# Kernel optimization log

Measured on AMD Instinct MI355X. Metric: run time of the kernel, lower is better.

Reference implementation:

```python
import jax, jax.numpy as jnp
import numpy as np

B, T, N, D, H, F, L, V = 4, 512, 1024, 384, 8, 1536, 6, 8000
HD = D // H


def _pe(t, d):
    pos = np.arange(t)[:, None].astype(np.float32)
    div = np.exp(np.arange(0, d, 2).astype(np.float32) * (-np.log(10000.0) / d))
    pe = np.zeros((t, d), np.float32)
    pe[:, 0::2] = np.sin(pos * div)
    pe[:, 1::2] = np.cos(pos * div)
    return jnp.asarray(pe)


def _ln(x, g, b, eps=1e-5):
    m = jnp.mean(x, -1, keepdims=True)
    v = jnp.mean((x - m) ** 2, -1, keepdims=True)
    return (x - m) * jax.lax.rsqrt(v + eps) * g + b


def _mha(xq, xkv, qw, qb, kw, kb, vw, vb, ow, ob, causal):
    Bq, Tq, Dm = xq.shape
    Nk = xkv.shape[1]

    def proj(x, w, b):
        return (x @ w + b).reshape(x.shape[0], x.shape[1], H, HD).transpose(0, 2, 1, 3)

    q, k, v = proj(xq, qw, qb), proj(xkv, kw, kb), proj(xkv, vw, vb)
    s = jnp.einsum('bhtd,bhnd->bhtn', q, k) * (HD ** -0.5)
    if causal:  # triu(ones(T, T_total), diagonal=1) since T_total == T (no cache)
        mask = jnp.triu(jnp.ones((Tq, Nk), bool), 1)
        s = jnp.where(mask, -jnp.inf, s)
    p = jax.nn.softmax(s, -1)
    o = jnp.einsum('bhtn,bhnd->bhtd', p, v).transpose(0, 2, 1, 3).reshape(Bq, Tq, Dm)
    return o @ ow + ob


def setup_inputs() -> dict:
    key = jax.random.key(0)
    ks = iter(jax.random.split(key, 40))
    w = lambda shape, s=0.02: jax.random.normal(next(ks), shape, jnp.float32) * s
    inp = {
        'encoder_out': jax.random.normal(next(ks), (B, N, D), jnp.float32),
        'emb': w((V, D)),
    }
    for p in ('sa', 'ca'):
        for n in ('q', 'k', 'v', 'o'):
            inp[f'{p}_{n}w'] = w((L, D, D))
            inp[f'{p}_{n}b'] = jnp.zeros((L, D), jnp.float32)
    for n in ('ln1', 'ln2', 'ln3'):
        inp[f'{n}_g'] = jnp.ones((L, D), jnp.float32)
        inp[f'{n}_b'] = jnp.zeros((L, D), jnp.float32)
    inp['ffn_w1'] = w((L, D, F)); inp['ffn_b1'] = jnp.zeros((L, F), jnp.float32)
    inp['ffn_w2'] = w((L, F, D)); inp['ffn_b2'] = jnp.zeros((L, D), jnp.float32)
    inp['on_g'] = jnp.ones((D,), jnp.float32); inp['on_b'] = jnp.zeros((D,), jnp.float32)
    inp['out_w'] = w((D, V)); inp['out_b'] = jnp.zeros((V,), jnp.float32)
    inp['target_ids'] = jax.random.randint(next(ks), (B, T), 0, V)
    return inp


def _forward(encoder_out, emb, sa_qw, sa_qb, sa_kw, sa_kb, sa_vw, sa_vb, sa_ow, sa_ob,
             ca_qw, ca_qb, ca_kw, ca_kb, ca_vw, ca_vb, ca_ow, ca_ob,
             ln1_g, ln1_b, ln2_g, ln2_b, ln3_g, ln3_b,
             ffn_w1, ffn_b1, ffn_w2, ffn_b2, on_g, on_b, out_w, out_b, target_ids):
    x = emb[target_ids] + _pe(T, D)[None]  # [B,T,D]
    for i in range(L):
        a = _mha(x, x, sa_qw[i], sa_qb[i], sa_kw[i], sa_kb[i], sa_vw[i], sa_vb[i], sa_ow[i], sa_ob[i], True)
        x = _ln(x + a, ln1_g[i], ln1_b[i])
        c = _mha(x, encoder_out, ca_qw[i], ca_qb[i], ca_kw[i], ca_kb[i], ca_vw[i], ca_vb[i], ca_ow[i], ca_ob[i], False)
        x = _ln(x + c, ln2_g[i], ln2_b[i])
        h = jax.nn.gelu(x @ ffn_w1[i] + ffn_b1[i], approximate=False) @ ffn_w2[i] + ffn_b2[i]
        x = _ln(x + h, ln3_g[i], ln3_b[i])
    x = _ln(x, on_g, on_b)
    return x @ out_w + out_b  # logits [B,T,V]


def reference(encoder_out, emb, sa_qw, sa_qb, sa_kw, sa_kb, sa_vw, sa_vb, sa_ow, sa_ob,
              ca_qw, ca_qb, ca_kw, ca_kb, ca_vw, ca_vb, ca_ow, ca_ob,
              ln1_g, ln1_b, ln2_g, ln2_b, ln3_g, ln3_b,
              ffn_w1, ffn_b1, ffn_w2, ffn_b2, on_g, on_b, out_w, out_b, target_ids):
    return _forward(encoder_out, emb, sa_qw, sa_qb, sa_kw, sa_kb, sa_vw, sa_vb, sa_ow, sa_ob,
                    ca_qw, ca_qb, ca_kw, ca_kb, ca_vw, ca_vb, ca_ow, ca_ob,
                    ln1_g, ln1_b, ln2_g, ln2_b, ln3_g, ln3_b,
                    ffn_w1, ffn_b1, ffn_w2, ffn_b2, on_g, on_b, out_w, out_b, target_ids)
```

## Files before the change

### kernel.cpp

```cpp
#include <hip/hip_runtime.h>
#include <hip/hip_bf16.h>
#include <math.h>

typedef __hip_bfloat16 bf16;
typedef __attribute__((ext_vector_type(8))) short short8;
typedef __attribute__((ext_vector_type(4))) float f32x4;
typedef __attribute__((ext_vector_type(4))) unsigned short us4;

#define Bc 4
#define Tc 512
#define Nc 1024
#define Dc 384
#define Hc 8
#define Fc 1536
#define Lc 6
#define Vc 8000
#define HDc 48

__device__ __forceinline__ float ldsel(const void* p, long long i, int isbf) {
  return isbf ? __bfloat162float(((const bf16*)p)[i]) : ((const float*)p)[i];
}
__device__ __forceinline__ void stsel(void* p, long long i, float v, int isbf) {
  if (isbf) ((bf16*)p)[i] = __float2bfloat16(v);
  else      ((float*)p)[i] = v;
}
__device__ __forceinline__ unsigned short f2bf(float x) {
  unsigned int u = __float_as_uint(x);
  return (unsigned short)((u + 0x7fffu + ((u >> 16) & 1u)) >> 16);
}

__global__ void detect_kernel(const unsigned int* __restrict__ g,
                              int* __restrict__ flag) {
  if (threadIdx.x == 0 && blockIdx.x == 0)
    *flag = (g[0] == 0x3F803F80u) ? 1 : 0;
}

__global__ __launch_bounds__(256) void wt_kernel(
    const void* __restrict__ in, bf16* __restrict__ out, int K, int N,
    long long outStride, const int* __restrict__ flagp) {
  const int isbf = *flagp;
  __shared__ float t[32][33];
  const long long cin = (long long)blockIdx.z * K * N;
  const long long cout = (long long)blockIdx.z * outStride;
  const int n0 = blockIdx.x * 32, k0 = blockIdx.y * 32;
  const int tx = threadIdx.x, ty = threadIdx.y;
#pragma unroll
  for (int r = 0; r < 4; ++r)
    t[ty * 4 + r][tx] =
        ldsel(in, cin + (long long)(k0 + ty * 4 + r) * N + n0 + tx, isbf);
  __syncthreads();
#pragma unroll
  for (int r = 0; r < 4; ++r)
    out[cout + (long long)(n0 + ty * 4 + r) * K + k0 + tx] =
        __float2bfloat16(t[tx][ty * 4 + r]);
}

__global__ __launch_bounds__(256) void cvt_kernel(
    const void* __restrict__ in, bf16* __restrict__ out,
    const int* __restrict__ flagp) {
  const int isbf = *flagp;
  const long long i = ((long long)blockIdx.x * 256 + threadIdx.x) * 4;
  if (isbf) {
    *(us4*)((unsigned short*)out + i) = *(const us4*)((const unsigned short*)in + i);
  } else {
    float4 v = *(const float4*)((const float*)in + i);
    unsigned short* o = (unsigned short*)out + i;
    o[0] = f2bf(v.x); o[1] = f2bf(v.y); o[2] = f2bf(v.z); o[3] = f2bf(v.w);
  }
}

__global__ __launch_bounds__(256) void bfuse_kernel(
    const void* __restrict__ b0, const void* __restrict__ b1,
    const void* __restrict__ b2, float* __restrict__ out, int nseg,
    const int* __restrict__ flagp) {
  const int isbf = *flagp;
  const int i = blockIdx.x;
  for (int n = threadIdx.x; n < Dc; n += 256) {
    out[(long long)i * nseg * Dc + n] = ldsel(b0, (long long)i * Dc + n, isbf);
    if (nseg > 1)
      out[(long long)i * nseg * Dc + Dc + n] = ldsel(b1, (long long)i * Dc + n, isbf);
    if (nseg > 2)
      out[(long long)i * nseg * Dc + 2 * Dc + n] = ldsel(b2, (long long)i * Dc + n, isbf);
  }
}

template <int BN>
__global__ __launch_bounds__(256) void mgemm128_kernel(
    const bf16* __restrict__ A, const bf16* __restrict__ Bt, long long bOff,
    const void* __restrict__ bias, long long biasOff, void* __restrict__ C,
    int M, int N, int K, int cMode, int act, int biasBf,
    const int* __restrict__ flagp) {
  constexpr int RN = BN / 32;
  const int isbf = *flagp;
  const int cbf = (cMode == 2) ? isbf : cMode;
  const int bbf = (biasBf == 2) ? isbf : biasBf;

  __shared__ __align__(16) unsigned short As[128][72];
  __shared__ __align__(16) unsigned short Bs[BN][72];

  const int tid = threadIdx.x;
  const int m0 = blockIdx.x * 128, n0 = blockIdx.y * BN;
  const int lane = tid & 63, wv = tid >> 6;
  const int wm = wv >> 1, wn = wv & 1;
  const int fr = lane & 15;
  const int fk = (lane >> 4) * 8;

  const int ar = tid >> 3;
  const int ac = (tid & 7) * 8;
  const bf16* Ap = A + (long long)(m0 + ar) * K + ac;
  const bf16* Bp = Bt + bOff + (long long)(n0 + ar) * K + ac;

  short8 pa[4], pb[RN * 2];
#pragma unroll
  for (int r = 0; r < 4; ++r) pa[r] = *(const short8*)(Ap + r * 32 * K);
#pragma unroll
  for (int r = 0; r < RN * 2; ++r) pb[r] = *(const short8*)(Bp + r * 32 * K);

  f32x4 acc[4][RN] = {};

  for (int k0 = 0; k0 < K; k0 += 64) {
#pragma unroll
    for (int r = 0; r < 4; ++r) *(short8*)(&As[ar + 32 * r][ac]) = pa[r];
#pragma unroll
    for (int r = 0; r < RN * 2; ++r) *(short8*)(&Bs[ar + 32 * r][ac]) = pb[r];
    __syncthreads();
    if (k0 + 64 < K) {
#pragma unroll
      for (int r = 0; r < 4; ++r)
        pa[r] = *(const short8*)(Ap + r * 32 * K + k0 + 64);
#pragma unroll
      for (int r = 0; r < RN * 2; ++r)
        pb[r] = *(const short8*)(Bp + r * 32 * K + k0 + 64);
    }
#pragma unroll
    for (int ks = 0; ks < 64; ks += 32) {
      short8 af[4];
#pragma unroll
      for (int mi = 0; mi < 4; ++mi)
        af[mi] = *(const short8*)(&As[wm * 64 + mi * 16 + fr][ks + fk]);
      short8 bg[RN];
#pragma unroll
      for (int ni = 0; ni < RN; ++ni)
        bg[ni] = *(const short8*)(&Bs[wn * (BN / 2) + ni * 16 + fr][ks + fk]);
#pragma unroll
      for (int mi = 0; mi < 4; ++mi)
#pragma unroll
        for (int ni = 0; ni < RN; ++ni)
          acc[mi][ni] =
              __builtin_amdgcn_mfma_f32_16x16x32_bf16(af[mi], bg[ni], acc[mi][ni], 0, 0, 0);
    }
    __syncthreads();
  }

#pragma unroll
  for (int ni = 0; ni < RN; ++ni) {
    const int col = n0 + wn * (BN / 2) + ni * 16 + fr;
    const float bv = bias ? ldsel(bias, biasOff + col, bbf) : 0.f;
#pragma unroll
    for (int mi = 0; mi < 4; ++mi) {
#pragma unroll
      for (int q = 0; q < 4; ++q) {
        const int row = m0 + wm * 64 + mi * 16 + (lane >> 4) * 4 + q;
        float v = acc[mi][ni][q] + bv;
        if (act == 1) v = 0.5f * v * (1.f + erff(v * 0.70710678118654752f));
        stsel(C, (long long)row * N + col, v, cbf);
      }
    }
  }
}

__global__ __launch_bounds__(256) void mgemm_kernel(
    const bf16* __restrict__ A, const void* __restrict__ B, long long bOff,
    const void* __restrict__ bias, long long biasOff, void* __restrict__ C,
    int M, int N, int K, int cMode, int act, int biasBf, int bT,
    const float* __restrict__ POm, const float* __restrict__ Mst,
    const float* __restrict__ Lst, int comb, const int* __restrict__ flagp) {
  const int isbf = *flagp;
  const int cbf = (cMode == 2) ? isbf : cMode;
  const int bbf = (biasBf == 2) ? isbf : biasBf;

  __shared__ __align__(16) unsigned short As[64][72];
  __shared__ __align__(16) unsigned short Bs[64][72];

  const int tid = threadIdx.x;
  const int m0 = blockIdx.x * 64, n0 = blockIdx.y * 64;
  const int lane = tid & 63, wv = tid >> 6;
  const int fr = lane & 15;
  const int fk = (lane >> 4) * 8;

  const int sr = tid >> 2;
  const int sk = (tid & 3) * 16;

  f32x4 acc[4] = {};

  if (bT == 0 && comb == 0) {
    const bf16* Bp = (const bf16*)B + bOff;
    const bf16* Ar = A + (long long)(m0 + sr) * K + sk;
    const bf16* Br = Bp + (long long)(n0 + sr) * K + sk;
    short8 a0 = *(const short8*)(Ar);
    short8 a1 = *(const short8*)(Ar + 8);
    short8 b0 = *(const short8*)(Br);
    short8 b1 = *(const short8*)(Br + 8);
    for (int k0 = 0; k0 < K; k0 += 64) {
      *(short8*)(&As[sr][sk]) = a0;
      *(short8*)(&As[sr][sk + 8]) = a1;
      *(short8*)(&Bs[sr][sk]) = b0;
      *(short8*)(&Bs[sr][sk + 8]) = b1;
      __syncthreads();
      if (k0 + 64 < K) {
        a0 = *(const short8*)(Ar + k0 + 64);
        a1 = *(const short8*)(Ar + k0 + 72);
        b0 = *(const short8*)(Br + k0 + 64);
        b1 = *(const short8*)(Br + k0 + 72);
      }
#pragma unroll
      for (int ks = 0; ks < 64; ks += 32) {
        short8 a = *(const short8*)(&As[16 * wv + fr][ks + fk]);
#pragma unroll
        for (int j = 0; j < 4; ++j) {
          short8 b = *(const short8*)(&Bs[16 * j + fr][ks + fk]);
          acc[j] = __builtin_amdgcn_mfma_f32_16x16x32_bf16(a, b, acc[j], 0, 0, 0);
        }
      }
      __syncthreads();
    }
  } else {
    const int bk = tid >> 2;
    const int bn = (tid & 3) * 16;
    for (int k0 = 0; k0 < K; k0 += 64) {
      if (comb) {
        const int gm = m0 + sr;
        const int gk = k0 + sk;
        const int hh = gk / 48;
        const int bb = gm >> 9, tt = gm & 511;
        const int mi = ((bb << 3) + hh) * 512 + tt;
        const float ma = Mst[mi], mb2 = Mst[16384 + mi];
        const float la = Lst[mi], lb2 = Lst[16384 + mi];
        const float MM = fmaxf(ma, mb2);
        float w0 = exp2f(ma - MM), w1 = exp2f(mb2 - MM);
        const float invL = 1.f / (w0 * la + w1 * lb2);
        w0 *= invL; w1 *= invL;
        const float* p0 = POm + (long long)gm * Dc + gk;
        const float* p1 = POm + (long long)(2048 + gm) * Dc + gk;
#pragma unroll
        for (int e = 0; e < 16; e += 4) {
          float4 x0 = *(const float4*)(p0 + e);
          float4 x1 = *(const float4*)(p1 + e);
          As[sr][sk + e + 0] = f2bf(w0 * x0.x + w1 * x1.x);
          As[sr][sk + e + 1] = f2bf(w0 * x0.y + w1 * x1.y);
          As[sr][sk + e + 2] = f2bf(w0 * x0.z + w1 * x1.z);
          As[sr][sk + e + 3] = f2bf(w0 * x0.w + w1 * x1.w);
        }
      } else {
        const long long off = (long long)(m0 + sr) * K + k0 + sk;
        const short8* p = (const short8*)(A + off);
        *(short8*)(&As[sr][sk]) = p[0];
        *(short8*)(&As[sr][sk + 8]) = p[1];
      }
      if (bT == 0) {
        const long long off = bOff + (long long)(n0 + sr) * K + k0 + sk;
        const short8* p = (const short8*)((const bf16*)B + off);
        *(short8*)(&Bs[sr][sk]) = p[0];
        *(short8*)(&Bs[sr][sk + 8]) = p[1];
      } else {
        const long long off = bOff + (long long)(k0 + bk) * N + n0 + bn;
        if (isbf) {
          const short8* p = (const short8*)((const bf16*)B + off);
          short8 v0 = p[0], v1 = p[1];
#pragma unroll
          for (int j = 0; j < 8; ++j) {
            Bs[bn + j][bk] = (unsigned short)v0[j];
            Bs[bn + 8 + j][bk] = (unsigned short)v1[j];
          }
        } else {
          const float4* p = (const float4*)((const float*)B + off);
          float4 f0 = p[0], f1 = p[1], f2 = p[2], f3 = p[3];
          Bs[bn + 0][bk] = f2bf(f0.x);  Bs[bn + 1][bk] = f2bf(f0.y);
          Bs[bn + 2][bk] = f2bf(f0.z);  Bs[bn + 3][bk] = f2bf(f0.w);
          Bs[bn + 4][bk] = f2bf(f1.x);  Bs[bn + 5][bk] = f2bf(f1.y);
          Bs[bn + 6][bk] = f2bf(f1.z);  Bs[bn + 7][bk] = f2bf(f1.w);
          Bs[bn + 8][bk] = f2bf(f2.x);  Bs[bn + 9][bk] = f2bf(f2.y);
          Bs[bn + 10][bk] = f2bf(f2.z); Bs[bn + 11][bk] = f2bf(f2.w);
          Bs[bn + 12][bk] = f2bf(f3.x); Bs[bn + 13][bk] = f2bf(f3.y);
          Bs[bn + 14][bk] = f2bf(f3.z); Bs[bn + 15][bk] = f2bf(f3.w);
        }
      }
      __syncthreads();
#pragma unroll
      for (int ks = 0; ks < 64; ks += 32) {
        short8 a = *(const short8*)(&As[16 * wv + fr][ks + fk]);
#pragma unroll
        for (int j = 0; j < 4; ++j) {
          short8 b = *(const short8*)(&Bs[16 * j + fr][ks + fk]);
          acc[j] = __builtin_amdgcn_mfma_f32_16x16x32_bf16(a, b, acc[j], 0, 0, 0);
        }
      }
      __syncthreads();
    }
  }

#pragma unroll
  for (int j = 0; j < 4; ++j) {
    const int col = n0 + 16 * j + fr;
    float bv = bias ? ldsel(bias, biasOff + col, bbf) : 0.f;
#pragma unroll
    for (int q = 0; q < 4; ++q) {
      const int row = m0 + 16 * wv + (lane >> 4) * 4 + q;
      float v = acc[j][q] + bv;
      if (act == 1) v = 0.5f * v * (1.f + erff(v * 0.70710678118654752f));
      stsel(C, (long long)row * N + col, v, cbf);
    }
  }
}

__global__ __launch_bounds__(256) void mattn_kernel(
    const bf16* __restrict__ Qb, int ldq, const bf16* __restrict__ Kb,
    const bf16* __restrict__ Vb, int ldkv, int kvRows,
    float* __restrict__ PO, float* __restrict__ Mb, float* __restrict__ Lb,
    int Nk, int causal) {
  const int bh = blockIdx.y;
  const int b = bh >> 3, h = bh & 7;
  const int row0 = blockIdx.x * 64;
  const int z = blockIdx.z;
  const int tid = threadIdx.x;
  const int lane = tid & 63, wv = tid >> 6;
  const int fr = lane & 15, g = lane >> 4;
  const int fk = g * 8, g4 = g * 4;
  const int rbase = row0 + wv * 16 + g4;

  __shared__ __align__(16) unsigned short Ks[64][72];
  __shared__ __align__(16) unsigned short Vt[48][72];
  __shared__ __align__(16) unsigned short Ps[4][16][72];

  for (int i = tid; i < 64 * 16; i += 256) Ks[i >> 4][48 + (i & 15)] = 0;

  const int qrow = row0 + wv * 16 + fr;
  const bf16* Qp = Qb + (long long)(b * Tc + qrow) * ldq + h * HDc;
  short8 q0 = *(const short8*)(Qp + fk);
  short8 q1 = {};
  if (g < 2) q1 = *(const short8*)(Qp + 32 + fk);

  const bf16* Kp = Kb + (long long)b * kvRows * ldkv + h * HDc;
  const bf16* Vp = Vb + (long long)b * kvRows * ldkv + h * HDc;

  const int c0 = tid, c1 = 256 + tid;
  const int r0 = c0 / 6, o0 = (c0 % 6) * 8;
  const int r1 = c1 / 6, o1 = (c1 % 6) * 8;
  const bool has1 = (tid < 128);

  const int nT = causal ? (blockIdx.x + 1) : (Nk >> 6);
  const int tlo = (nT * z) >> 1, thi = (nT * (z + 1)) >> 1;

  float m[4] = {-3e38f, -3e38f, -3e38f, -3e38f};
  float l[4] = {0.f, 0.f, 0.f, 0.f};
  f32x4 oa[3] = {};

  short8 kA = {}, vA = {}, kB = {}, vB = {};
  if (tlo < thi) {
    const long long nb = (long long)tlo * 64;
    kA = *(const short8*)(Kp + (nb + r0) * ldkv + o0);
    vA = *(const short8*)(Vp + (nb + r0) * ldkv + o0);
    if (has1) {
      kB = *(const short8*)(Kp + (nb + r1) * ldkv + o1);
      vB = *(const short8*)(Vp + (nb + r1) * ldkv + o1);
    }
  }

  const float scale = 0.20823509f;

  for (int t = tlo; t < thi; ++t) {
    *(short8*)&Ks[r0][o0] = kA;
#pragma unroll
    for (int j = 0; j < 8; ++j) Vt[o0 + j][r0] = (unsigned short)vA[j];
    if (has1) {
      *(short8*)&Ks[r1][o1] = kB;
#pragma unroll
      for (int j = 0; j < 8; ++j) Vt[o1 + j][r1] = (unsigned short)vB[j];
    }
    __syncthreads();

    if (t + 1 < thi) {
      const long long nb = (long long)(t + 1) * 64;
      kA = *(const short8*)(Kp + (nb + r0) * ldkv + o0);
      vA = *(const short8*)(Vp + (nb + r0) * ldkv + o0);
      if (has1) {
        kB = *(const short8*)(Kp + (nb + r1) * ldkv + o1);
        vB = *(const short8*)(Vp + (nb + r1) * ldkv + o1);
      }
    }

    f32x4 s[4] = {};
#pragma unroll
    for (int tt = 0; tt < 4; ++tt) {
      short8 b0 = *(const short8*)&Ks[16 * tt + fr][fk];
      short8 b1 = *(const short8*)&Ks[16 * tt + fr][32 + fk];
      s[tt] = __builtin_amdgcn_mfma_f32_16x16x32_bf16(q0, b0, s[tt], 0, 0, 0);
      s[tt] = __builtin_amdgcn_mfma_f32_16x16x32_bf16(q1, b1, s[tt], 0, 0, 0);
    }

    const int n0 = t * 64;
#pragma unroll
    for (int tt = 0; tt < 4; ++tt) {
      const int n = n0 + 16 * tt + fr;
#pragma unroll
      for (int q = 0; q < 4; ++q) {
        float v = s[tt][q] * scale;
        if (causal && n > rbase + q) v = -3e38f;
        s[tt][q] = v;
      }
    }

#pragma unroll
    for (int q = 0; q < 4; ++q) {
      float tm = fmaxf(fmaxf(s[0][q], s[1][q]), fmaxf(s[2][q], s[3][q]));
      tm = fmaxf(tm, __shfl_xor(tm, 1, 64));
      tm = fmaxf(tm, __shfl_xor(tm, 2, 64));
      tm = fmaxf(tm, __shfl_xor(tm, 4, 64));
      tm = fmaxf(tm, __shfl_xor(tm, 8, 64));
      const float mn = fmaxf(m[q], tm);
      const float f = exp2f(m[q] - mn);
      float rs = 0.f;
#pragma unroll
      for (int tt = 0; tt < 4; ++tt) {
        float p = exp2f(s[tt][q] - mn);
        s[tt][q] = p;
        rs += p;
      }
      rs += __shfl_xor(rs, 1, 64);
      rs += __shfl_xor(rs, 2, 64);
      rs += __shfl_xor(rs, 4, 64);
      rs += __shfl_xor(rs, 8, 64);
      l[q] = l[q] * f + rs;
      m[q] = mn;
      oa[0][q] *= f;
      oa[1][q] *= f;
      oa[2][q] *= f;
    }

#pragma unroll
    for (int tt = 0; tt < 4; ++tt)
#pragma unroll
      for (int q = 0; q < 4; ++q)
        Ps[wv][g4 + q][16 * tt + fr] = f2bf(s[tt][q]);

#pragma unroll
    for (int ks = 0; ks < 64; ks += 32) {
      short8 a = *(const short8*)&Ps[wv][fr][ks + fk];
#pragma unroll
      for (int jd = 0; jd < 3; ++jd) {
        short8 bv = *(const short8*)&Vt[16 * jd + fr][ks + fk];
        oa[jd] = __builtin_amdgcn_mfma_f32_16x16x32_bf16(a, bv, oa[jd], 0, 0, 0);
      }
    }
    __syncthreads();
  }

#pragma unroll
  for (int q = 0; q < 4; ++q) {
    float* pp = PO + (long long)(z * (Bc * Tc) + b * Tc + rbase + q) * Dc + h * HDc;
#pragma unroll
    for (int jd = 0; jd < 3; ++jd) pp[16 * jd + fr] = oa[jd][q];
    if (fr == 0) {
      const int mi = z * (Bc * Hc * Tc) + (bh << 9) + rbase + q;
      Mb[mi] = m[q];
      Lb[mi] = l[q];
    }
  }
}

__global__ __launch_bounds__(256) void lnw_kernel(
    const float* __restrict__ X, const float* __restrict__ R,
    const void* __restrict__ g, const void* __restrict__ bta, long long gOff,
    void* __restrict__ Y, int yMode, bf16* __restrict__ Yb,
    const int* __restrict__ flagp) {
  const int isbf = *flagp;
  const long long row = blockIdx.x * 4 + (threadIdx.x >> 6);
  const int lane = threadIdx.x & 63;
  const float* xr = X + row * Dc;
  const float* rr = R ? R + row * Dc : nullptr;
  float v[6];
  float s = 0.f, s2 = 0.f;
#pragma unroll
  for (int j = 0; j < 6; ++j) {
    const int d = lane + 64 * j;
    float x = xr[d] + (rr ? rr[d] : 0.f);
    v[j] = x; s += x; s2 += x * x;
  }
#pragma unroll
  for (int k = 1; k < 64; k <<= 1) {
    s += __shfl_xor(s, k, 64);
    s2 += __shfl_xor(s2, k, 64);
  }
  const float mean = s * (1.f / 384.f);
  const float var = s2 * (1.f / 384.f) - mean * mean;
  const float rstd = rsqrtf(var + 1e-5f);
  const long long yo = row * Dc;
#pragma unroll
  for (int j = 0; j < 6; ++j) {
    const int d = lane + 64 * j;
    float y = (v[j] - mean) * rstd * ldsel(g, gOff + d, isbf) +
              ldsel(bta, gOff + d, isbf);
    stsel(Y, yo + d, y, yMode);
    if (Yb) Yb[yo + d] = __float2bfloat16(y);
  }
}

__global__ __launch_bounds__(384) void embed_kernel(
    const void* __restrict__ emb, const int* __restrict__ ids,
    float* __restrict__ X, bf16* __restrict__ Xb,
    const int* __restrict__ flagp) {
  const int isbf = *flagp;
  long long row = blockIdx.x;
  int t = (int)(row % Tc);
  int d = threadIdx.x;
  int id = ids[row];
  float e = ldsel(emb, (long long)id * Dc + d, isbf);
  int i2 = d & ~1;
  float div = expf((float)i2 * (-9.210340371976184f / 384.f));
  float ang = (float)t * div;
  float pe = (d & 1) ? cosf(ang) : sinf(ang);
  float v = e + pe;
  X[row * Dc + d] = v;
  Xb[row * Dc + d] = __float2bfloat16(v);
}

extern "C" void kernel_launch(void* const* d_in, const int* in_sizes, int n_in,
                              void* d_out, int out_size, void* d_ws,
                              size_t ws_size, hipStream_t stream) {
  (void)in_sizes; (void)n_in; (void)out_size;

  const void* enc = d_in[0];
  const void* emb = d_in[1];
  const void* sa_w[4]; const void* sa_b[4];
  for (int j = 0; j < 4; ++j) { sa_w[j] = d_in[2 + 2 * j]; sa_b[j] = d_in[3 + 2 * j]; }
  const void* ca_w[4]; const void* ca_b[4];
  for (int j = 0; j < 4; ++j) { ca_w[j] = d_in[10 + 2 * j]; ca_b[j] = d_in[11 + 2 * j]; }
  const void* ln_g[3]; const void* ln_b[3];
  for (int j = 0; j < 3; ++j) { ln_g[j] = d_in[18 + 2 * j]; ln_b[j] = d_in[19 + 2 * j]; }
  const void* fw1 = d_in[24];
  const void* fb1 = d_in[25];
  const void* fw2 = d_in[26];
  const void* fb2 = d_in[27];
  const void* ong = d_in[28];
  const void* onb = d_in[29];
  const void* outw = d_in[30];
  const void* outb = d_in[31];
  const int* ids = (const int*)d_in[32];

  char* ob = (char*)d_out;
  float* X   = (float*)ob;
  bf16* Xb   = (bf16*)(ob + 3145728);
  float* AO  = (float*)(ob + 4718592);
  bf16* QKV  = (bf16*)(ob + 7864320);
  bf16* KVca = (bf16*)(ob + 12582912);
  bf16* HID  = (bf16*)(ob + 20447232);
  float* PO  = (float*)(ob + 20447232);
  float* Mb  = (float*)(ob + 26738688);
  float* Lb  = (float*)(ob + 26869760);
  bf16* encB = (bf16*)(ob + 27000832);
  float* bQKV = (float*)(ob + 30146560);
  float* bKVc = (float*)(ob + 30174208);

  bf16* Y = (bf16*)d_ws;
  int* flag = (int*)((char*)d_ws + 1572864);

  const bool bigws = (ws_size >= (size_t)36028672);
  char* wtb = (char*)d_ws + 1573120;
  bf16* saQKVT = (bf16*)(wtb + 0);
  bf16* saOT   = (bf16*)(wtb + 5308416);
  bf16* caQT   = (bf16*)(wtb + 7077888);
  bf16* caKVT  = (bf16*)(wtb + 8847360);
  bf16* caOT   = (bf16*)(wtb + 12386304);
  bf16* f1T    = (bf16*)(wtb + 14155776);
  bf16* f2T    = (bf16*)(wtb + 21233664);
  bf16* outT   = (bf16*)(wtb + 28311552);

  const int BT = Bc * Tc;
  const int F32 = 0, BF16 = 1, FLAG = 2;

  detect_kernel<<<dim3(1), dim3(64), 0, stream>>>((const unsigned int*)ln_g[0], flag);

  if (bigws) {
    auto wt = [&](const void* in, bf16* out, int K, int N, long long ostr, int C) {
      wt_kernel<<<dim3(N / 32, K / 32, C), dim3(32, 8), 0, stream>>>(
          in, out, K, N, ostr, flag);
    };
    wt(sa_w[0], saQKVT, 384, 384, 1152LL * 384, Lc);
    wt(sa_w[1], saQKVT + 147456, 384, 384, 1152LL * 384, Lc);
    wt(sa_w[2], saQKVT + 294912, 384, 384, 1152LL * 384, Lc);
    wt(sa_w[3], saOT, 384, 384, 147456, Lc);
    wt(ca_w[0], caQT, 384, 384, 147456, Lc);
    wt(ca_w[1], caKVT, 384, 384, 294912, Lc);
    wt(ca_w[2], caKVT + 147456, 384, 384, 294912, Lc);
    wt(ca_w[3], caOT, 384, 384, 147456, Lc);
    wt(fw1, f1T, 384, 1536, 589824, Lc);
    wt(fw2, f2T, 1536, 384, 589824, Lc);
    wt(outw, outT, 384, 8000, 0, 1);
    bfuse_kernel<<<dim3(Lc), dim3(256), 0, stream>>>(sa_b[0], sa_b[1], sa_b[2],
                                                     bQKV, 3, flag);
    bfuse_kernel<<<dim3(Lc), dim3(256), 0, stream>>>(ca_b[1], ca_b[2], ca_b[2],
                                                     bKVc, 2, flag);
  }
  cvt_kernel<<<dim3(1536), dim3(256), 0, stream>>>(enc, encB, flag);

  auto gemm128 = [&](const bf16* A, const bf16* Bt, long long bOff,
                     const void* bias, long long biasOff, int biasBf, void* C,
                     int M, int N, int K, int cM, int act) {
    mgemm128_kernel<128><<<dim3(M / 128, N / 128), dim3(256), 0, stream>>>(
        A, Bt, bOff, bias, biasOff, C, M, N, K, cM, act, biasBf, flag);
  };
  auto gemm128n64 = [&](const bf16* A, const bf16* Bt, long long bOff,
                        const void* bias, long long biasOff, int biasBf,
                        void* C, int M, int N, int K, int cM, int act) {
    mgemm128_kernel<64><<<dim3(M / 128, N / 64), dim3(256), 0, stream>>>(
        A, Bt, bOff, bias, biasOff, C, M, N, K, cM, act, biasBf, flag);
  };
  auto gemmOld = [&](const bf16* A, const void* Bo, long long bOff,
                     const void* bias, long long biasOff, int biasBf, void* C,
                     int M, int N, int K, int cM, int act, int bT, int comb) {
    mgemm_kernel<<<dim3(M / 64, N / 64), dim3(256), 0, stream>>>(
        A, Bo, bOff, bias, biasOff, C, M, N, K, cM, act, biasBf, bT,
        PO, Mb, Lb, comb, flag);
  };
  auto ln = [&](const float* Xp, const float* Rp, const void* g,
                const void* b, long long gOff, void* Yp, int yMode, bf16* Yb) {
    lnw_kernel<<<dim3(BT / 4), dim3(256), 0, stream>>>(Xp, Rp, g, b, gOff, Yp,
                                                       yMode, Yb, flag);
  };
  auto attn = [&](const bf16* Q, int ldq, const bf16* Kp, const bf16* Vp,
                  int ldkv, int kvRows, int Nk, int causal) {
    mattn_kernel<<<dim3(Tc / 64, Bc * Hc, 2), dim3(256), 0, stream>>>(
        Q, ldq, Kp, Vp, ldkv, kvRows, PO, Mb, Lb, Nk, causal);
  };

  embed_kernel<<<dim3(BT), dim3(384), 0, stream>>>(emb, ids, X, Xb, flag);

  bf16* Qf = QKV;
  bf16* Kf = KVca;
  bf16* Vf = (bf16*)((char*)KVca + 3145728);

  for (int i = 0; i < Lc; ++i) {
    const long long wD = (long long)i * Dc * Dc;
    const long long bD = (long long)i * Dc;

    if (bigws) {
      gemm128(Xb, saQKVT, (long long)i * 1152 * 384, bQKV, (long long)i * 1152,
              F32, QKV, BT, 1152, 384, BF16, 0);
      attn(QKV, 1152, QKV + 384, QKV + 768, 1152, Tc, Tc, 1);
      gemmOld(nullptr, saOT, wD, sa_b[3], bD, FLAG, AO, BT, Dc, Dc, F32, 0, 0, 1);
    } else {
      gemmOld(Xb, sa_w[0], wD, sa_b[0], bD, FLAG, Qf, BT, Dc, Dc, BF16, 0, 1, 0);
      gemmOld(Xb, sa_w[1], wD, sa_b[1], bD, FLAG, Kf, BT, Dc, Dc, BF16, 0, 1, 0);
      gemmOld(Xb, sa_w[2], wD, sa_b[2], bD, FLAG, Vf, BT, Dc, Dc, BF16, 0, 1, 0);
      attn(Qf, 384, Kf, Vf, 384, Tc, Tc, 1);
      gemmOld(nullptr, sa_w[3], wD, sa_b[3], bD, FLAG, AO, BT, Dc, Dc, F32, 0, 1, 1);
    }
    ln(X, AO, ln_g[0], ln_b[0], bD, X, F32, Xb);

    if (bigws) {
      gemmOld(Xb, caQT, wD, ca_b[0], bD, FLAG, QKV, BT, Dc, Dc, BF16, 0, 0, 0);
      gemm128(encB, caKVT, (long long)i * 768 * 384, bKVc, (long long)i * 768,
              F32, KVca, Bc * Nc, 768, 384, BF16, 0);
      attn(QKV, 384, KVca, KVca + 384, 768, Nc, Nc, 0);
      gemmOld(nullptr, caOT, wD, ca_b[3], bD, FLAG, AO, BT, Dc, Dc, F32, 0, 0, 1);
    } else {
      gemmOld(Xb, ca_w[0], wD, ca_b[0], bD, FLAG, Qf, BT, Dc, Dc, BF16, 0, 1, 0);
      gemmOld(encB, ca_w[1], wD, ca_b[1], bD, FLAG, Kf, Bc * Nc, Dc, Dc, BF16, 0, 1, 0);
      gemmOld(encB, ca_w[2], wD, ca_b[2], bD, FLAG, Vf, Bc * Nc, Dc, Dc, BF16, 0, 1, 0);
      attn(Qf, 384, Kf, Vf, 384, Nc, Nc, 0);
      gemmOld(nullptr, ca_w[3], wD, ca_b[3], bD, FLAG, AO, BT, Dc, Dc, F32, 0, 1, 1);
    }
    ln(X, AO, ln_g[1], ln_b[1], bD, X, F32, Xb);

    if (bigws) {
      gemm128(Xb, f1T, (long long)i * 1536 * 384, fb1, (long long)i * Fc, FLAG,
              HID, BT, Fc, Dc, BF16, 1 );
      gemmOld(HID, f2T, (long long)i * 384 * 1536, fb2, bD, FLAG, AO,
              BT, Dc, Fc, F32, 0, 0, 0);
    } else {
      gemmOld(Xb, fw1, (long long)i * Dc * Fc, fb1, (long long)i * Fc, FLAG,
              HID, BT, Fc, Dc, BF16, 1, 1, 0);
      gemmOld(HID, fw2, (long long)i * Fc * Dc, fb2, bD, FLAG, AO,
              BT, Dc, Fc, F32, 0, 1, 0);
    }
    ln(X, AO, ln_g[2], ln_b[2], bD, X, F32, Xb);
  }

  ln(X, nullptr, ong, onb, 0, Y, BF16, nullptr);
  if (bigws)
    gemm128n64(Y, outT, 0, outb, 0, FLAG, d_out, BT, Vc, Dc, FLAG, 0);
  else
    gemmOld(Y, outw, 0, outb, 0, FLAG, d_out, BT, Vc, Dc, FLAG, 0, 1, 0);
}
```

Measured before the change: 1.154 ms.

## Split attention combine into separate kernel and add XCD-aware block swizzle

Moves the split-KV attention combine (softmax rescaling of two partial outputs) out of the output-projection GEMM's A-tile loader into a standalone acomb kernel that writes a bf16 attention buffer, so the O-projection GEMM can use the fast prefetching bf16 path. It also remaps block indices in both GEMM kernels so that consecutive tiles land on the same XCD, for better L2 locality. The cost is an extra kernel launch and a bf16 round trip through memory for each attention call.

```diff
diff --git a/kernel.cpp b/kernel.cpp
--- a/kernel.cpp
+++ b/kernel.cpp
@@ -27,6 +27,12 @@
 __device__ __forceinline__ unsigned short f2bf(float x) {
   unsigned int u = __float_as_uint(x);
   return (unsigned short)((u + 0x7fffu + ((u >> 16) & 1u)) >> 16);
+}
+
+__device__ __forceinline__ int xcd_swz(int d, int nwg) {
+  const int q = nwg >> 3, r = nwg & 7;
+  const int x = d & 7, idx = d >> 3;
+  return (x < r) ? x * (q + 1) + idx : r * (q + 1) + (x - r) * q + idx;
 }
 
 __global__ void detect_kernel(const unsigned int* __restrict__ g,
@@ -99,7 +105,9 @@
   __shared__ __align__(16) unsigned short Bs[BN][72];
 
   const int tid = threadIdx.x;
-  const int m0 = blockIdx.x * 128, n0 = blockIdx.y * BN;
+  const int gx = gridDim.x;
+  const int wl = xcd_swz(blockIdx.y * gx + blockIdx.x, gx * gridDim.y);
+  const int m0 = (wl % gx) * 128, n0 = (wl / gx) * BN;
   const int lane = tid & 63, wv = tid >> 6;
   const int wm = wv >> 1, wn = wv & 1;
   const int fr = lane & 15;
@@ -173,8 +181,7 @@
     const bf16* __restrict__ A, const void* __restrict__ B, long long bOff,
     const void* __restrict__ bias, long long biasOff, void* __restrict__ C,
     int M, int N, int K, int cMode, int act, int biasBf, int bT,
-    const float* __restrict__ POm, const float* __restrict__ Mst,
-    const float* __restrict__ Lst, int comb, const int* __restrict__ flagp) {
+    const int* __restrict__ flagp) {
   const int isbf = *flagp;
   const int cbf = (cMode == 2) ? isbf : cMode;
   const int bbf = (biasBf == 2) ? isbf : biasBf;
@@ -183,7 +190,9 @@
   __shared__ __align__(16) unsigned short Bs[64][72];
 
   const int tid = threadIdx.x;
-  const int m0 = blockIdx.x * 64, n0 = blockIdx.y * 64;
+  const int gx = gridDim.x;
+  const int wl = xcd_swz(blockIdx.y * gx + blockIdx.x, gx * gridDim.y);
+  const int m0 = (wl % gx) * 64, n0 = (wl / gx) * 64;
   const int lane = tid & 63, wv = tid >> 6;
   const int fr = lane & 15;
   const int fk = (lane >> 4) * 8;
@@ -193,7 +202,7 @@
 
   f32x4 acc[4] = {};
 
-  if (bT == 0 && comb == 0) {
+  if (bT == 0) {
     const bf16* Bp = (const bf16*)B + bOff;
     const bf16* Ar = A + (long long)(m0 + sr) * K + sk;
     const bf16* Br = Bp + (long long)(n0 + sr) * K + sk;
@@ -228,62 +237,32 @@
     const int bk = tid >> 2;
     const int bn = (tid & 3) * 16;
     for (int k0 = 0; k0 < K; k0 += 64) {
-      if (comb) {
-        const int gm = m0 + sr;
-        const int gk = k0 + sk;
-        const int hh = gk / 48;
-        const int bb = gm >> 9, tt = gm & 511;
-        const int mi = ((bb << 3) + hh) * 512 + tt;
-        const float ma = Mst[mi], mb2 = Mst[16384 + mi];
-        const float la = Lst[mi], lb2 = Lst[16384 + mi];
-        const float MM = fmaxf(ma, mb2);
-        float w0 = exp2f(ma - MM), w1 = exp2f(mb2 - MM);
-        const float invL = 1.f / (w0 * la + w1 * lb2);
-        w0 *= invL; w1 *= invL;
-        const float* p0 = POm + (long long)gm * Dc + gk;
-        const float* p1 = POm + (long long)(2048 + gm) * Dc + gk;
-#pragma unroll
-        for (int e = 0; e < 16; e += 4) {
-          float4 x0 = *(const float4*)(p0 + e);
-          float4 x1 = *(const float4*)(p1 + e);
-          As[sr][sk + e + 0] = f2bf(w0 * x0.x + w1 * x1.x);
-          As[sr][sk + e + 1] = f2bf(w0 * x0.y + w1 * x1.y);
-          As[sr][sk + e + 2] = f2bf(w0 * x0.z + w1 * x1.z);
-          As[sr][sk + e + 3] = f2bf(w0 * x0.w + w1 * x1.w);
-        }
-      } else {
+      {
         const long long off = (long long)(m0 + sr) * K + k0 + sk;
         const short8* p = (const short8*)(A + off);
         *(short8*)(&As[sr][sk]) = p[0];
         *(short8*)(&As[sr][sk + 8]) = p[1];
       }
-      if (bT == 0) {
-        const long long off = bOff + (long long)(n0 + sr) * K + k0 + sk;
+      const long long off = bOff + (long long)(k0 + bk) * N + n0 + bn;
+      if (isbf) {
         const short8* p = (const short8*)((const bf16*)B + off);
-        *(short8*)(&Bs[sr][sk]) = p[0];
-        *(short8*)(&Bs[sr][sk + 8]) = p[1];
+        short8 v0 = p[0], v1 = p[1];
+#pragma unroll
+        for (int j = 0; j < 8; ++j) {
+          Bs[bn + j][bk] = (unsigned short)v0[j];
+          Bs[bn + 8 + j][bk] = (unsigned short)v1[j];
+        }
       } else {
-        const long long off = bOff + (long long)(k0 + bk) * N + n0 + bn;
-        if (isbf) {
-          const short8* p = (const short8*)((const bf16*)B + off);
-          short8 v0 = p[0], v1 = p[1];
-#pragma unroll
-          for (int j = 0; j < 8; ++j) {
-            Bs[bn + j][bk] = (unsigned short)v0[j];
-            Bs[bn + 8 + j][bk] = (unsigned short)v1[j];
-          }
-        } else {
-          const float4* p = (const float4*)((const float*)B + off);
-          float4 f0 = p[0], f1 = p[1], f2 = p[2], f3 = p[3];
-          Bs[bn + 0][bk] = f2bf(f0.x);  Bs[bn + 1][bk] = f2bf(f0.y);
-          Bs[bn + 2][bk] = f2bf(f0.z);  Bs[bn + 3][bk] = f2bf(f0.w);
-          Bs[bn + 4][bk] = f2bf(f1.x);  Bs[bn + 5][bk] = f2bf(f1.y);
-          Bs[bn + 6][bk] = f2bf(f1.z);  Bs[bn + 7][bk] = f2bf(f1.w);
-          Bs[bn + 8][bk] = f2bf(f2.x);  Bs[bn + 9][bk] = f2bf(f2.y);
-          Bs[bn + 10][bk] = f2bf(f2.z); Bs[bn + 11][bk] = f2bf(f2.w);
-          Bs[bn + 12][bk] = f2bf(f3.x); Bs[bn + 13][bk] = f2bf(f3.y);
-          Bs[bn + 14][bk] = f2bf(f3.z); Bs[bn + 15][bk] = f2bf(f3.w);
-        }
+        const float4* p = (const float4*)((const float*)B + off);
+        float4 f0 = p[0], f1 = p[1], f2 = p[2], f3 = p[3];
+        Bs[bn + 0][bk] = f2bf(f0.x);  Bs[bn + 1][bk] = f2bf(f0.y);
+        Bs[bn + 2][bk] = f2bf(f0.z);  Bs[bn + 3][bk] = f2bf(f0.w);
+        Bs[bn + 4][bk] = f2bf(f1.x);  Bs[bn + 5][bk] = f2bf(f1.y);
+        Bs[bn + 6][bk] = f2bf(f1.z);  Bs[bn + 7][bk] = f2bf(f1.w);
+        Bs[bn + 8][bk] = f2bf(f2.x);  Bs[bn + 9][bk] = f2bf(f2.y);
+        Bs[bn + 10][bk] = f2bf(f2.z); Bs[bn + 11][bk] = f2bf(f2.w);
+        Bs[bn + 12][bk] = f2bf(f3.x); Bs[bn + 13][bk] = f2bf(f3.y);
+        Bs[bn + 14][bk] = f2bf(f3.z); Bs[bn + 15][bk] = f2bf(f3.w);
       }
       __syncthreads();
 #pragma unroll
@@ -466,6 +445,24 @@
       Lb[mi] = l[q];
     }
   }
+}
+
+__global__ __launch_bounds__(384) void acomb_kernel(
+    const float* __restrict__ PO, const float* __restrict__ Mb,
+    const float* __restrict__ Lb, bf16* __restrict__ ATT) {
+  const int row = blockIdx.x;
+  const int d = threadIdx.x;
+  const int b = row >> 9, t = row & 511;
+  const int h = d / HDc;
+  const int mi = ((b << 3) + h) * Tc + t;
+  const float m0 = Mb[mi], m1 = Mb[Bc * Hc * Tc + mi];
+  const float l0 = Lb[mi], l1 = Lb[Bc * Hc * Tc + mi];
+  const float M = fmaxf(m0, m1);
+  const float w0 = exp2f(m0 - M), w1 = exp2f(m1 - M);
+  const float L = w0 * l0 + w1 * l1;
+  const float o = (w0 * PO[(long long)row * Dc + d] +
+                   w1 * PO[(long long)(Bc * Tc + row) * Dc + d]) / L;
+  ATT[(long long)row * Dc + d] = __float2bfloat16(o);
 }
 
 __global__ __launch_bounds__(256) void lnw_kernel(
@@ -553,6 +550,7 @@
   float* AO  = (float*)(ob + 4718592);
   bf16* QKV  = (bf16*)(ob + 7864320);
   bf16* KVca = (bf16*)(ob + 12582912);
+  bf16* ATT  = (bf16*)(ob + 18874368);
   bf16* HID  = (bf16*)(ob + 20447232);
   float* PO  = (float*)(ob + 20447232);
   float* Mb  = (float*)(ob + 26738688);
@@ -615,12 +613,17 @@
     mgemm128_kernel<64><<<dim3(M / 128, N / 64), dim3(256), 0, stream>>>(
         A, Bt, bOff, bias, biasOff, C, M, N, K, cM, act, biasBf, flag);
   };
-  auto gemmOld = [&](const bf16* A, const void* Bo, long long bOff,
-                     const void* bias, long long biasOff, int biasBf, void* C,
-                     int M, int N, int K, int cM, int act, int bT, int comb) {
+  auto gemmT = [&](const bf16* A, const bf16* Bt, long long bOff,
+                   const void* bias, long long biasOff, int biasBf, void* C,
+                   int M, int N, int K, int cM, int act) {
     mgemm_kernel<<<dim3(M / 64, N / 64), dim3(256), 0, stream>>>(
-        A, Bo, bOff, bias, biasOff, C, M, N, K, cM, act, biasBf, bT,
-        PO, Mb, Lb, comb, flag);
+        A, Bt, bOff, bias, biasOff, C, M, N, K, cM, act, biasBf, 0, flag);
+  };
+  auto gemmO = [&](const bf16* A, const void* Bo, long long bOff,
+                   const void* bias, long long biasOff, void* C,
+                   int M, int N, int K, int cM, int act) {
+    mgemm_kernel<<<dim3(M / 64, N / 64), dim3(256), 0, stream>>>(
+        A, Bo, bOff, bias, biasOff, C, M, N, K, cM, act, FLAG, 1, flag);
   };
   auto ln = [&](const float* Xp, const float* Rp, const void* g,
                 const void* b, long long gOff, void* Yp, int yMode, bf16* Yb) {
@@ -631,6 +634,7 @@
                   int ldkv, int kvRows, int Nk, int causal) {
     mattn_kernel<<<dim3(Tc / 64, Bc * Hc, 2), dim3(256), 0, stream>>>(
         Q, ldq, Kp, Vp, ldkv, kvRows, PO, Mb, Lb, Nk, causal);
+    acomb_kernel<<<dim3(BT), dim3(384), 0, stream>>>(PO, Mb, Lb, ATT);
   };
 
   embed_kernel<<<dim3(BT), dim3(384), 0, stream>>>(emb, ids, X, Xb, flag);
@@ -647,41 +651,40 @@
       gemm128(Xb, saQKVT, (long long)i * 1152 * 384, bQKV, (long long)i * 1152,
               F32, QKV, BT, 1152, 384, BF16, 0);
       attn(QKV, 1152, QKV + 384, QKV + 768, 1152, Tc, Tc, 1);
-      gemmOld(nullptr, saOT, wD, sa_b[3], bD, FLAG, AO, BT, Dc, Dc, F32, 0, 0, 1);
+      gemmT(ATT, saOT, wD, sa_b[3], bD, FLAG, AO, BT, Dc, Dc, F32, 0);
     } else {
-      gemmOld(Xb, sa_w[0], wD, sa_b[0], bD, FLAG, Qf, BT, Dc, Dc, BF16, 0, 1, 0);
-      gemmOld(Xb, sa_w[1], wD, sa_b[1], bD, FLAG, Kf, BT, Dc, Dc, BF16, 0, 1, 0);
-      gemmOld(Xb, sa_w[2], wD, sa_b[2], bD, FLAG, Vf, BT, Dc, Dc, BF16, 0, 1, 0);
+      gemmO(Xb, sa_w[0], wD, sa_b[0], bD, Qf, BT, Dc, Dc, BF16, 0);
+      gemmO(Xb, sa_w[1], wD, sa_b[1], bD, Kf, BT, Dc, Dc, BF16, 0);
+      gemmO(Xb, sa_w[2], wD, sa_b[2], bD, Vf, BT, Dc, Dc, BF16, 0);
       attn(Qf, 384, Kf, Vf, 384, Tc, Tc, 1);
-      gemmOld(nullptr, sa_w[3], wD, sa_b[3], bD, FLAG, AO, BT, Dc, Dc, F32, 0, 1, 1);
+      gemmO(ATT, sa_w[3], wD, sa_b[3], bD, AO, BT, Dc, Dc, F32, 0);
     }
     ln(X, AO, ln_g[0], ln_b[0], bD, X, F32, Xb);
 
     if (bigws) {
-      gemmOld(Xb, caQT, wD, ca_b[0], bD, FLAG, QKV, BT, Dc, Dc, BF16, 0, 0, 0);
+      gemmT(Xb, caQT, wD, ca_b[0], bD, FLAG, QKV, BT, Dc, Dc, BF16, 0);
       gemm128(encB, caKVT, (long long)i * 768 * 384, bKVc, (long long)i * 768,
               F32, KVca, Bc * Nc, 768, 384, BF16, 0);
       attn(QKV, 384, KVca, KVca + 384, 768, Nc, Nc, 0);
-      gemmOld(nullptr, caOT, wD, ca_b[3], bD, FLAG, AO, BT, Dc, Dc, F32, 0, 0, 1);
+      gemmT(ATT, caOT, wD, ca_b[3], bD, FLAG, AO, BT, Dc, Dc, F32, 0);
     } else {
-      gemmOld(Xb, ca_w[0], wD, ca_b[0], bD, FLAG, Qf, BT, Dc, Dc, BF16, 0, 1, 0);
-      gemmOld(encB, ca_w[1], wD, ca_b[1], bD, FLAG, Kf, Bc * Nc, Dc, Dc, BF16, 0, 1, 0);
-      gemmOld(encB, ca_w[2], wD, ca_b[2], bD, FLAG, Vf, Bc * Nc, Dc, Dc, BF16, 0, 1, 0);
+      gemmO(Xb, ca_w[0], wD, ca_b[0], bD, Qf, BT, Dc, Dc, BF16, 0);
+      gemmO(encB, ca_w[1], wD, ca_b[1], bD, Kf, Bc * Nc, Dc, Dc, BF16, 0);
+      gemmO(encB, ca_w[2], wD, ca_b[2], bD, Vf, Bc * Nc, Dc, Dc, BF16, 0);
       attn(Qf, 384, Kf, Vf, 384, Nc, Nc, 0);
-      gemmOld(nullptr, ca_w[3], wD, ca_b[3], bD, FLAG, AO, BT, Dc, Dc, F32, 0, 1, 1);
+      gemmO(ATT, ca_w[3], wD, ca_b[3], bD, AO, BT, Dc, Dc, F32, 0);
     }
     ln(X, AO, ln_g[1], ln_b[1], bD, X, F32, Xb);
 
     if (bigws) {
       gemm128(Xb, f1T, (long long)i * 1536 * 384, fb1, (long long)i * Fc, FLAG,
               HID, BT, Fc, Dc, BF16, 1 );
-      gemmOld(HID, f2T, (long long)i * 384 * 1536, fb2, bD, FLAG, AO,
-              BT, Dc, Fc, F32, 0, 0, 0);
+      gemmT(HID, f2T, (long long)i * 384 * 1536, fb2, bD, FLAG, AO,
+            BT, Dc, Fc, F32, 0);
     } else {
-      gemmOld(Xb, fw1, (long long)i * Dc * Fc, fb1, (long long)i * Fc, FLAG,
-              HID, BT, Fc, Dc, BF16, 1, 1, 0);
-      gemmOld(HID, fw2, (long long)i * Fc * Dc, fb2, bD, FLAG, AO,
-              BT, Dc, Fc, F32, 0, 1, 0);
+      gemmO(Xb, fw1, (long long)i * Dc * Fc, fb1, (long long)i * Fc, HID,
+            BT, Fc, Dc, BF16, 1);
+      gemmO(HID, fw2, (long long)i * Fc * Dc, fb2, bD, AO, BT, Dc, Fc, F32, 0);
     }
     ln(X, AO, ln_g[2], ln_b[2], bD, X, F32, Xb);
   }
@@ -690,5 +693,5 @@
   if (bigws)
     gemm128n64(Y, outT, 0, outb, 0, FLAG, d_out, BT, Vc, Dc, FLAG, 0);
   else
-    gemmOld(Y, outw, 0, outb, 0, FLAG, d_out, BT, Vc, Dc, FLAG, 0, 1, 0);
-}
+    gemmO(Y, outw, 0, outb, 0, d_out, BT, Vc, Dc, FLAG, 0);
+}
```

After: 1.160 ms. About the same (+0.5%).
